# Performance work log

Measured on AMD Instinct MI355X. Metric: run time of the kernel, lower is better.

Reference implementation:

```python
import jax, jax.numpy as jnp
import numpy as np

B, N_FEAT, SEQ, E, H, V = 32, 196, 64, 1024, 1024, 32000


def setup_inputs() -> dict:
    key = jax.random.key(0)
    ks = jax.random.split(key, 16)
    s = 0.02
    return {
        "features": jax.random.normal(ks[0], (B, N_FEAT, E), jnp.float32),
        "captions": jax.random.randint(ks[1], (B, SEQ), 0, V),
        "max_seq_length": SEQ,
        # decoder embedding table (vocab, embed)
        "emb": jax.random.normal(ks[2], (V, E), jnp.float32) * s,
        # attention MLP: Linear(E->H), Tanh, Linear(H->1)
        "Wa1": jax.random.normal(ks[3], (H, E), jnp.float32) * s,
        "ba1": jnp.zeros((H,), jnp.float32),
        "Wa2": jax.random.normal(ks[4], (1, H), jnp.float32) * s,
        "ba2": jnp.zeros((1,), jnp.float32),
        # GRU (1 layer), input = concat(word_emb, context) -> E + H
        "W_ih": jax.random.normal(ks[5], (3 * H, E + H), jnp.float32) * s,
        "W_hh": jax.random.normal(ks[6], (3 * H, H), jnp.float32) * s,
        "b_ih": jnp.zeros((3 * H,), jnp.float32),
        "b_hh": jnp.zeros((3 * H,), jnp.float32),
        # output projection Linear(H -> V)
        "W_fc": jax.random.normal(ks[7], (V, H), jnp.float32) * s,
        "b_fc": jnp.zeros((V,), jnp.float32),
    }


def reference(features, captions, max_seq_length, emb, Wa1, ba1, Wa2, ba2,
              W_ih, W_hh, b_ih, b_hh, W_fc, b_fc):
    # words: (B, S, E)
    words = emb[captions]
    # combined: (B, N_FEAT + S, E)
    combined = jnp.concatenate([features, words], axis=1)
    # attention scores over the combined tokens, softmax along token axis
    scores = jnp.tanh(combined @ Wa1.T + ba1) @ Wa2.T + ba2   # (B, M, 1)
    A = jax.nn.softmax(scores, axis=1)                         # (B, M, 1)
    # context h0 = A^T @ combined -> (B, E); used both as GRU h0 and per-step context
    h0 = jnp.sum(A * combined, axis=1)
    context = h0

    def gru_cell(x, h):
        gi = x @ W_ih.T + b_ih          # (B, 3H)
        gh = h @ W_hh.T + b_hh          # (B, 3H)
        ir, iz, inn = jnp.split(gi, 3, axis=-1)
        hr, hz, hn = jnp.split(gh, 3, axis=-1)
        r = jax.nn.sigmoid(ir + hr)
        z = jax.nn.sigmoid(iz + hz)
        n = jnp.tanh(inn + r * hn)
        return (1.0 - z) * n + z * h

    def step(carry, _):
        input_word, h = carry
        x = jnp.concatenate([emb[input_word], context], axis=-1)  # (B, E+H)
        h_new = gru_cell(x, h)
        out = h_new @ W_fc.T + b_fc                               # (B, V)
        # greedy feedback (eval path / no teacher forcing)
        next_word = jnp.argmax(out, axis=-1)
        return (next_word, h_new), out

    init = (captions[:, 0], h0)
    (_, _), outs = jax.lax.scan(step, init, None, length=max_seq_length - 1)
    outs = jnp.transpose(outs, (1, 0, 2))                         # (B, S-1, V)
    bsz = captions.shape[0]
    vocab = W_fc.shape[0]
    outputs = jnp.concatenate(
        [jnp.zeros((bsz, 1, vocab), outs.dtype), outs], axis=1)   # t=0 stays zero
    return outputs, A
```

## Files before the change

kernel.cpp:

```cpp
#include <hip/hip_runtime.h>
#include <hip/hip_bf16.h>

typedef unsigned long long ull;
typedef unsigned int uint;

#define NB 32
#define NFEAT 196
#define SEQL 64
#define ED 1024
#define HD 1024
#define VOC 32000
#define NCOMB 260
#define NROWS (NB*NCOMB)
#define NTILE 2000

typedef __attribute__((ext_vector_type(8))) short s16x8;
typedef __attribute__((ext_vector_type(4))) float f32x4;
typedef __attribute__((ext_vector_type(4))) uint  u32x4;

union FragU { u32x4 u; s16x8 s; };

#define DOT4(acc, wv, xv) acc = fmaf((wv).x,(xv).x, fmaf((wv).y,(xv).y, fmaf((wv).z,(xv).z, fmaf((wv).w,(xv).w,(acc)))))

__device__ __forceinline__ uint enc_f32(float f) {
    uint u = __float_as_uint(f);
    return (u & 0x80000000u) ? ~u : (u | 0x80000000u);
}
__device__ __forceinline__ ull shflxor64(ull v, int m) {
    uint lo = __shfl_xor((uint)v, m);
    uint hi = __shfl_xor((uint)(v >> 32), m);
    return (((ull)hi) << 32) | (ull)lo;
}

__device__ __forceinline__ void split2(float a, float b, uint& hi, uint& lo) {
    __hip_bfloat162 h2 = __float22bfloat162_rn(make_float2(a, b));
    float2 hf = __bfloat1622float2(h2);
    __hip_bfloat162 l2 = __float22bfloat162_rn(make_float2(a - hf.x, b - hf.y));
    hi = *(uint*)&h2;
    lo = *(uint*)&l2;
}

__device__ __forceinline__ void nt_store4(float* p, float a, float b, float c, float d) {
    f32x4 v = {a, b, c, d};
    __builtin_nontemporal_store(v, (f32x4*)p);
}

__global__ void __launch_bounds__(256) k_build(
    const float* __restrict__ features, const int* __restrict__ captions,
    const float* __restrict__ emb, float* __restrict__ combined,
    float* __restrict__ out)
{
    const int bid = blockIdx.x;
    const int t = threadIdx.x;
    if (bid < NROWS) {
        const int b = bid / NCOMB;
        const int i = bid - b*NCOMB;
        const float* src = (i < NFEAT)
            ? (features + ((size_t)(b*NFEAT + i))*ED)
            : (emb + (size_t)captions[b*SEQL + (i - NFEAT)]*ED);
        float4* dst4 = (float4*)(combined + (size_t)bid*ED);
        const float4* s4 = (const float4*)src;
        dst4[t] = s4[t];
    } else {
        const int z = bid - NROWS;
        const int m = z*1024 + t*4;
        if (m < NB*VOC) {
            const int b = m / VOC;
            const int v = m - b*VOC;
            nt_store4(out + (size_t)b*((size_t)SEQL*VOC) + v, 0.f, 0.f, 0.f, 0.f);
        }
    }
}

__global__ void __launch_bounds__(256) k_pack_w1(
    const float* __restrict__ Wa1, uint* __restrict__ W1hi, uint* __restrict__ W1lo)
{
    const int eid = blockIdx.x*256 + threadIdx.x;
    const int lane = eid & 63;
    const int ks = (eid >> 6) & 31;
    const int ct = eid >> 11;
    const int c = ct*16 + (lane & 15);
    const int k0 = ks*32 + ((lane >> 4) & 3)*4;
    const float4 wa = *(const float4*)&Wa1[(size_t)c*ED + k0];
    const float4 wb = *(const float4*)&Wa1[(size_t)c*ED + k0 + 16];
    uint hi[4], lo[4];
    split2(wa.x, wa.y, hi[0], lo[0]);
    split2(wa.z, wa.w, hi[1], lo[1]);
    split2(wb.x, wb.y, hi[2], lo[2]);
    split2(wb.z, wb.w, hi[3], lo[3]);
    *(u32x4*)&W1hi[(size_t)eid*4] = (u32x4){hi[0], hi[1], hi[2], hi[3]};
    *(u32x4*)&W1lo[(size_t)eid*4] = (u32x4){lo[0], lo[1], lo[2], lo[3]};
}

__global__ void __launch_bounds__(256) k_pack_wfc(
    const float* __restrict__ W_fc, uint* __restrict__ Whi, uint* __restrict__ Wlo)
{
    const int eid = blockIdx.x*256 + threadIdx.x;
    const int lane = eid & 63;
    const int ks = (eid >> 6) & 31;
    const int tile = eid >> 11;
    const int row = tile*16 + (lane & 15);
    const int k0 = ks*32 + ((lane >> 4) & 3)*4;
    const float4 wa = *(const float4*)&W_fc[(size_t)row*HD + k0];
    const float4 wb = *(const float4*)&W_fc[(size_t)row*HD + k0 + 16];
    uint hi[4], lo[4];
    split2(wa.x, wa.y, hi[0], lo[0]);
    split2(wa.z, wa.w, hi[1], lo[1]);
    split2(wb.x, wb.y, hi[2], lo[2]);
    split2(wb.z, wb.w, hi[3], lo[3]);
    *(u32x4*)&Whi[(size_t)eid*4] = (u32x4){hi[0], hi[1], hi[2], hi[3]};
    *(u32x4*)&Wlo[(size_t)eid*4] = (u32x4){lo[0], lo[1], lo[2], lo[3]};
}

__global__ void __launch_bounds__(256) k_attn_mfma(
    const float* __restrict__ combined, const uint* __restrict__ W1hi,
    const uint* __restrict__ W1lo, const float* __restrict__ ba1,
    const float* __restrict__ Wa2, float* __restrict__ partials)
{
    const int t = threadIdx.x;
    const int w = t >> 6, l = t & 63;
    const int lane16 = l & 15, qk = (l >> 4) & 3;
    const int rt = blockIdx.x*4 + w;
    const int cg0 = blockIdx.y*2;

    const float* Arow = combined + (size_t)(rt*16 + lane16)*ED;
    const u32x4* bh_base = (const u32x4*)W1hi + l;
    const u32x4* bl_base = (const u32x4*)W1lo + l;

    f32x4 acc[2][4];
#pragma unroll
    for (int c = 0; c < 2; ++c)
#pragma unroll
        for (int i = 0; i < 4; ++i) acc[c][i] = (f32x4){0.f,0.f,0.f,0.f};

#pragma unroll 2
    for (int ks = 0; ks < 32; ++ks) {
        const int k0 = ks*32 + qk*4;
        const float4 aa = *(const float4*)(Arow + k0);
        const float4 ab = *(const float4*)(Arow + k0 + 16);
        FragU ahi, alo;
        uint h0,l0_,h1,l1_,h2,l2_,h3,l3_;
        split2(aa.x, aa.y, h0, l0_);
        split2(aa.z, aa.w, h1, l1_);
        split2(ab.x, ab.y, h2, l2_);
        split2(ab.z, ab.w, h3, l3_);
        ahi.u = (u32x4){h0, h1, h2, h3};
        alo.u = (u32x4){l0_, l1_, l2_, l3_};
#pragma unroll
        for (int c = 0; c < 2; ++c) {
#pragma unroll
            for (int i = 0; i < 4; ++i) {
                const size_t idx = (((size_t)((cg0 + c)*4 + i))*32 + ks)*64;
                FragU bh_, bl_;
                bh_.u = bh_base[idx];
                bl_.u = bl_base[idx];
                acc[c][i] = __builtin_amdgcn_mfma_f32_16x16x32_bf16(ahi.s, bh_.s, acc[c][i], 0, 0, 0);
                acc[c][i] = __builtin_amdgcn_mfma_f32_16x16x32_bf16(ahi.s, bl_.s, acc[c][i], 0, 0, 0);
                acc[c][i] = __builtin_amdgcn_mfma_f32_16x16x32_bf16(alo.s, bh_.s, acc[c][i], 0, 0, 0);
            }
        }
    }

#pragma unroll
    for (int c = 0; c < 2; ++c) {
        const int cg = cg0 + c;
        float s[4];
#pragma unroll
        for (int r = 0; r < 4; ++r) {
            float sum = 0.f;
#pragma unroll
            for (int i = 0; i < 4; ++i) {
                const int col = cg*64 + i*16 + lane16;
                sum += tanhf(acc[c][i][r] + ba1[col]) * Wa2[col];
            }
            s[r] = sum;
        }
#pragma unroll
        for (int m = 1; m <= 8; m <<= 1)
#pragma unroll
            for (int r = 0; r < 4; ++r) s[r] += __shfl_xor(s[r], m);
        if (lane16 == 0) {
#pragma unroll
            for (int r = 0; r < 4; ++r)
                partials[(size_t)(rt*16 + qk*4 + r)*16 + cg] = s[r];
        }
    }
}

__global__ void __launch_bounds__(256) k_attn_finish(
    const float* __restrict__ partials, const float* __restrict__ combined,
    const int* __restrict__ captions,
    float* __restrict__ A_out, float* __restrict__ h0,
    float* __restrict__ ctx, ull* __restrict__ slots0)
{
    const int b = blockIdx.x, t = threadIdx.x;
    __shared__ float sc[NCOMB];
    __shared__ float red[256];

    for (int i = t; i < NCOMB; i += 256) {
        float s = 0.f;
        const float* pr = partials + (size_t)(b*NCOMB + i)*16;
#pragma unroll
        for (int g = 0; g < 16; ++g) s += pr[g];
        sc[i] = s;
    }
    __syncthreads();
    float m = -1e30f;
    for (int i = t; i < NCOMB; i += 256) m = fmaxf(m, sc[i]);
    red[t] = m; __syncthreads();
    for (int s2 = 128; s2 > 0; s2 >>= 1) {
        if (t < s2) red[t] = fmaxf(red[t], red[t+s2]);
        __syncthreads();
    }
    m = red[0]; __syncthreads();
    float ssum = 0.f;
    for (int i = t; i < NCOMB; i += 256) { float e = expf(sc[i] - m); sc[i] = e; ssum += e; }
    red[t] = ssum; __syncthreads();
    for (int s2 = 128; s2 > 0; s2 >>= 1) {
        if (t < s2) red[t] += red[t+s2];
        __syncthreads();
    }
    const float S = red[0]; __syncthreads();
    for (int i = t; i < NCOMB; i += 256) {
        const float a = sc[i] / S;
        sc[i] = a;
        A_out[b*NCOMB + i] = a;
    }
    __syncthreads();
    for (int e = t; e < HD; e += 256) {
        float acc = 0.f;
        const float* cb = combined + (size_t)b*NCOMB*ED + e;
        for (int i = 0; i < NCOMB; ++i) acc = fmaf(sc[i], cb[(size_t)i*ED], acc);
        h0[(size_t)b*HD + e] = acc;
        ctx[(size_t)b*HD + e] = acc;
    }
    if (t == 0) {
        slots0[0*NB + b] = (ull)(~(uint)captions[b*SEQL]);
#pragma unroll
        for (int g = 1; g < 8; ++g) slots0[g*NB + b] = 0ull;
    }
}

__global__ void __launch_bounds__(256) k_gictx(
    const float* __restrict__ W_ih, const float* __restrict__ b_ih,
    const float* __restrict__ ctx, float* __restrict__ gictx)
{
    const int jj = blockIdx.x;
    const int t = threadIdx.x;
    const int w = t >> 6, l = t & 63;
    const int b0 = w*8;
    const float* Wrow = W_ih + (size_t)jj*(ED+HD) + ED;

    float a[8];
#pragma unroll
    for (int i = 0; i < 8; ++i) a[i] = 0.f;
#pragma unroll
    for (int q = 0; q < 4; ++q) {
        const int k = q*256 + l*4;
        const float4 wv = *(const float4*)(Wrow + k);
#pragma unroll
        for (int i = 0; i < 8; ++i) {
            const float4 xv = *(const float4*)(ctx + (size_t)(b0 + i)*HD + k);
            DOT4(a[i], wv, xv);
        }
    }
    int s = (l >> 5) & 1;
    int ib = s*4;
    float tA[4];
#pragma unroll
    for (int ii = 0; ii < 4; ++ii) {
        const float send = a[(1^s)*4 + ii];
        tA[ii] = a[s*4 + ii] + __shfl_xor(send, 32);
    }
    s = (l >> 4) & 1; ib += s*2;
    float tB[2];
#pragma unroll
    for (int jj2 = 0; jj2 < 2; ++jj2) {
        const float send = tA[(1^s)*2 + jj2];
        tB[jj2] = tA[s*2 + jj2] + __shfl_xor(send, 16);
    }
    s = (l >> 3) & 1; ib += s;
    float fg;
    {
        const float send = tB[1^s];
        fg = tB[s] + __shfl_xor(send, 8);
    }
#pragma unroll
    for (int mm = 4; mm >= 1; mm >>= 1) fg += __shfl_xor(fg, mm);
    if ((l & 7) == 0)
        gictx[(size_t)jj*NB + (b0 + ib)] = fg + b_ih[jj];
}

__global__ void __launch_bounds__(256) k_gru(
    const float* __restrict__ emb, const float* __restrict__ W_ih,
    const float* __restrict__ W_hh, const float* __restrict__ gictx,
    const float* __restrict__ b_hh,
    const float* __restrict__ h_prev, float* __restrict__ h_next,
    const ull* __restrict__ slots_prev, ull* __restrict__ slots_cur,
    uint* __restrict__ Hhi, uint* __restrict__ Hlo)
{
    __shared__ int word_s[NB];
    const int t = threadIdx.x;
    if (t < NB) {
        ull best = 0ull;
#pragma unroll
        for (int g = 0; g < 8; ++g) {
            ull k = slots_prev[g*NB + t];
            best = (k > best) ? k : best;
        }
        word_s[t] = (int)(~(uint)best);
    }
    if (blockIdx.x == 0) slots_cur[t] = 0ull;
    __syncthreads();

    const int j = blockIdx.x;
    const int w = t >> 6, l = t & 63;
    const int b0 = w*8;

    float a[4][8];
#pragma unroll
    for (int g = 0; g < 4; ++g)
#pragma unroll
        for (int i = 0; i < 8; ++i) a[g][i] = 0.f;

    const float* Wr = W_ih + (size_t)j*(ED+HD);
    const float* Wz = W_ih + (size_t)(HD + j)*(ED+HD);
    const float* Wn = W_ih + (size_t)(2*HD + j)*(ED+HD);
#pragma unroll
    for (int q = 0; q < 4; ++q) {
        const int k = q*256 + l*4;
        const float4 wr = *(const float4*)(Wr + k);
        const float4 wz = *(const float4*)(Wz + k);
        const float4 wn = *(const float4*)(Wn + k);
#pragma unroll
        for (int i = 0; i < 8; ++i) {
            const float4 xv = *(const float4*)(emb + (size_t)word_s[b0+i]*ED + k);
            DOT4(a[0][i], wr, xv);
            DOT4(a[1][i], wz, xv);
            DOT4(a[2][i], wn, xv);
        }
    }
    const float* Ur = W_hh + (size_t)j*HD;
    const float* Uz = W_hh + (size_t)(HD + j)*HD;
    const float* Un = W_hh + (size_t)(2*HD + j)*HD;
#pragma unroll
    for (int q = 0; q < 4; ++q) {
        const int k = q*256 + l*4;
        const float4 ur = *(const float4*)(Ur + k);
        const float4 uz = *(const float4*)(Uz + k);
        const float4 un = *(const float4*)(Un + k);
#pragma unroll
        for (int i = 0; i < 8; ++i) {
            const float4 hv = *(const float4*)(h_prev + (size_t)(b0+i)*HD + k);
            DOT4(a[0][i], ur, hv);
            DOT4(a[1][i], uz, hv);
            DOT4(a[3][i], un, hv);
        }
    }
    int s = (l >> 5) & 1;
    int ib = s*4;
    float tA[4][4];
#pragma unroll
    for (int g = 0; g < 4; ++g)
#pragma unroll
        for (int ii = 0; ii < 4; ++ii) {
            const float send = a[g][(1^s)*4 + ii];
            tA[g][ii] = a[g][s*4 + ii] + __shfl_xor(send, 32);
        }
    s = (l >> 4) & 1; ib += s*2;
    float tB[4][2];
#pragma unroll
    for (int g = 0; g < 4; ++g)
#pragma unroll
        for (int jj = 0; jj < 2; ++jj) {
            const float send = tA[g][(1^s)*2 + jj];
            tB[g][jj] = tA[g][s*2 + jj] + __shfl_xor(send, 16);
        }
    s = (l >> 3) & 1; ib += s;
    float fg[4];
#pragma unroll
    for (int g = 0; g < 4; ++g) {
        const float send = tB[g][1^s];
        fg[g] = tB[g][s] + __shfl_xor(send, 8);
    }
#pragma unroll
    for (int mm = 4; mm >= 1; mm >>= 1)
#pragma unroll
        for (int g = 0; g < 4; ++g) fg[g] += __shfl_xor(fg[g], mm);

    if ((l & 7) == 0) {
        const int b = b0 + ib;
        const float gcr = gictx[(size_t)j*NB + b];
        const float gcz = gictx[(size_t)(HD + j)*NB + b];
        const float gcn = gictx[(size_t)(2*HD + j)*NB + b];
        const float rg = 1.f/(1.f + expf(-(fg[0] + gcr + b_hh[j])));
        const float zg = 1.f/(1.f + expf(-(fg[1] + gcz + b_hh[HD+j])));
        const float ng = tanhf(fg[2] + gcn + rg*(fg[3] + b_hh[2*HD+j]));
        const float hp = h_prev[(size_t)b*HD + j];
        const float hv = (1.f - zg)*ng + zg*hp;
        h_next[(size_t)b*HD + j] = hv;
        __hip_bfloat16 hb = __float2bfloat16(hv);
        const float hf = __bfloat162float(hb);
        __hip_bfloat16 lb = __float2bfloat16(hv - hf);
        const int bh = b >> 4;
        const int ks = j >> 5;
        const int qk2 = (j >> 2) & 3;
        const int elem = (j & 3) + 4*((j >> 4) & 1);
        const size_t ei = (((size_t)(bh*32 + ks))*64 + qk2*16 + (b & 15))*8 + elem;
        ((ushort*)Hhi)[ei] = *(const ushort*)&hb;
        ((ushort*)Hlo)[ei] = *(const ushort*)&lb;
    }
}

__global__ void __launch_bounds__(256) k_logits(
    const float* __restrict__ W_fc, const uint* __restrict__ Wfchi,
    const uint* __restrict__ Wfclo, const uint* __restrict__ Hhi,
    const uint* __restrict__ Hlo, const float* __restrict__ b_fc,
    float* __restrict__ out, ull* __restrict__ slots_cur, int tstep, int packed)
{
    __shared__ float sm[32][68];
    __shared__ float mergebuf[2][64][16];
    const int t = threadIdx.x;
    const int w = t >> 6, l = t & 63;
    const int lane16 = l & 15, qk = (l >> 4) & 3;
    const int tp = w & 1;
    const int kh = w >> 1;
    const int tile0 = blockIdx.x*4 + tp*2;

    const u32x4* hh0 = (const u32x4*)Hhi + (size_t)(kh*16)*64 + l;
    const u32x4* hl0 = (const u32x4*)Hlo + (size_t)(kh*16)*64 + l;
    const u32x4* hh1 = (const u32x4*)Hhi + (size_t)(32 + kh*16)*64 + l;
    const u32x4* hl1 = (const u32x4*)Hlo + (size_t)(32 + kh*16)*64 + l;

    f32x4 accA0 = {0.f,0.f,0.f,0.f};
    f32x4 accA1 = {0.f,0.f,0.f,0.f};
    f32x4 accB0 = {0.f,0.f,0.f,0.f};
    f32x4 accB1 = {0.f,0.f,0.f,0.f};

    if (packed) {
        const u32x4* WHa = (const u32x4*)Wfchi + ((size_t)tile0*32 + kh*16)*64 + l;
        const u32x4* WLa = (const u32x4*)Wfclo + ((size_t)tile0*32 + kh*16)*64 + l;
        const u32x4* WHb = WHa + (size_t)32*64;
        const u32x4* WLb = WLa + (size_t)32*64;
#pragma unroll 2
        for (int ks = 0; ks < 16; ++ks) {
            FragU wha, wla, whb, wlb, b0h, b0l, b1h, b1l;
            wha.u = WHa[ks*64];
            wla.u = WLa[ks*64];
            whb.u = WHb[ks*64];
            wlb.u = WLb[ks*64];
            b0h.u = hh0[ks*64];
            b0l.u = hl0[ks*64];
            b1h.u = hh1[ks*64];
            b1l.u = hl1[ks*64];
            accA0 = __builtin_amdgcn_mfma_f32_16x16x32_bf16(wha.s, b0h.s, accA0, 0, 0, 0);
            accA0 = __builtin_amdgcn_mfma_f32_16x16x32_bf16(wha.s, b0l.s, accA0, 0, 0, 0);
            accA0 = __builtin_amdgcn_mfma_f32_16x16x32_bf16(wla.s, b0h.s, accA0, 0, 0, 0);
            accA1 = __builtin_amdgcn_mfma_f32_16x16x32_bf16(wha.s, b1h.s, accA1, 0, 0, 0);
            accA1 = __builtin_amdgcn_mfma_f32_16x16x32_bf16(wha.s, b1l.s, accA1, 0, 0, 0);
            accA1 = __builtin_amdgcn_mfma_f32_16x16x32_bf16(wla.s, b1h.s, accA1, 0, 0, 0);
            accB0 = __builtin_amdgcn_mfma_f32_16x16x32_bf16(whb.s, b0h.s, accB0, 0, 0, 0);
            accB0 = __builtin_amdgcn_mfma_f32_16x16x32_bf16(whb.s, b0l.s, accB0, 0, 0, 0);
            accB0 = __builtin_amdgcn_mfma_f32_16x16x32_bf16(wlb.s, b0h.s, accB0, 0, 0, 0);
            accB1 = __builtin_amdgcn_mfma_f32_16x16x32_bf16(whb.s, b1h.s, accB1, 0, 0, 0);
            accB1 = __builtin_amdgcn_mfma_f32_16x16x32_bf16(whb.s, b1l.s, accB1, 0, 0, 0);
            accB1 = __builtin_amdgcn_mfma_f32_16x16x32_bf16(wlb.s, b1h.s, accB1, 0, 0, 0);
        }
    } else {
        const float* WrowA = W_fc + (size_t)(tile0*16 + lane16)*HD;
        const float* WrowB = W_fc + (size_t)((tile0 + 1)*16 + lane16)*HD;
#pragma unroll 2
        for (int ks = 0; ks < 16; ++ks) {
            const int k0 = (kh*16 + ks)*32 + qk*4;
            const float4 waA = *(const float4*)(WrowA + k0);
            const float4 wbA = *(const float4*)(WrowA + k0 + 16);
            const float4 waB = *(const float4*)(WrowB + k0);
            const float4 wbB = *(const float4*)(WrowB + k0 + 16);
            FragU wha, wla, whb, wlb;
            uint h0,l0_,h1,l1_,h2,l2_,h3,l3_;
            split2(waA.x, waA.y, h0, l0_);
            split2(waA.z, waA.w, h1, l1_);
            split2(wbA.x, wbA.y, h2, l2_);
            split2(wbA.z, wbA.w, h3, l3_);
            wha.u = (u32x4){h0, h1, h2, h3};
            wla.u = (u32x4){l0_, l1_, l2_, l3_};
            split2(waB.x, waB.y, h0, l0_);
            split2(waB.z, waB.w, h1, l1_);
            split2(wbB.x, wbB.y, h2, l2_);
            split2(wbB.z, wbB.w, h3, l3_);
            whb.u = (u32x4){h0, h1, h2, h3};
            wlb.u = (u32x4){l0_, l1_, l2_, l3_};
            FragU b0h, b0l, b1h, b1l;
            b0h.u = hh0[ks*64];
            b0l.u = hl0[ks*64];
            b1h.u = hh1[ks*64];
            b1l.u = hl1[ks*64];
            accA0 = __builtin_amdgcn_mfma_f32_16x16x32_bf16(wha.s, b0h.s, accA0, 0, 0, 0);
            accA0 = __builtin_amdgcn_mfma_f32_16x16x32_bf16(wha.s, b0l.s, accA0, 0, 0, 0);
            accA0 = __builtin_amdgcn_mfma_f32_16x16x32_bf16(wla.s, b0h.s, accA0, 0, 0, 0);
            accA1 = __builtin_amdgcn_mfma_f32_16x16x32_bf16(wha.s, b1h.s, accA1, 0, 0, 0);
            accA1 = __builtin_amdgcn_mfma_f32_16x16x32_bf16(wha.s, b1l.s, accA1, 0, 0, 0);
            accA1 = __builtin_amdgcn_mfma_f32_16x16x32_bf16(wla.s, b1h.s, accA1, 0, 0, 0);
            accB0 = __builtin_amdgcn_mfma_f32_16x16x32_bf16(whb.s, b0h.s, accB0, 0, 0, 0);
            accB0 = __builtin_amdgcn_mfma_f32_16x16x32_bf16(whb.s, b0l.s, accB0, 0, 0, 0);
            accB0 = __builtin_amdgcn_mfma_f32_16x16x32_bf16(wlb.s, b0h.s, accB0, 0, 0, 0);
            accB1 = __builtin_amdgcn_mfma_f32_16x16x32_bf16(whb.s, b1h.s, accB1, 0, 0, 0);
            accB1 = __builtin_amdgcn_mfma_f32_16x16x32_bf16(whb.s, b1l.s, accB1, 0, 0, 0);
            accB1 = __builtin_amdgcn_mfma_f32_16x16x32_bf16(wlb.s, b1h.s, accB1, 0, 0, 0);
        }
    }

    if (kh == 1) {
        float* rr = &mergebuf[tp][l][0];
        *(float4*)&rr[0]  = make_float4(accA0[0], accA0[1], accA0[2], accA0[3]);
        *(float4*)&rr[4]  = make_float4(accA1[0], accA1[1], accA1[2], accA1[3]);
        *(float4*)&rr[8]  = make_float4(accB0[0], accB0[1], accB0[2], accB0[3]);
        *(float4*)&rr[12] = make_float4(accB1[0], accB1[1], accB1[2], accB1[3]);
    }
    __syncthreads();
    if (kh == 0) {
        const float* rr = &mergebuf[tp][l][0];
        const float4 biasA = *(const float4*)&b_fc[tile0*16 + qk*4];
        const float4 biasB = *(const float4*)&b_fc[(tile0 + 1)*16 + qk*4];
#pragma unroll
        for (int r = 0; r < 4; ++r) {
            const int rlocA = tp*32 + qk*4 + r;
            const int rlocB = tp*32 + 16 + qk*4 + r;
            const float bA = (&biasA.x)[r];
            const float bB = (&biasB.x)[r];
            sm[lane16][rlocA]      = accA0[r] + rr[r]      + bA;
            sm[16 + lane16][rlocA] = accA1[r] + rr[4 + r]  + bA;
            sm[lane16][rlocB]      = accB0[r] + rr[8 + r]  + bB;
            sm[16 + lane16][rlocB] = accB1[r] + rr[12 + r] + bB;
        }
    }
    __syncthreads();
    {
        const int b = t >> 3;
        const int rl0 = (t & 7)*8;
        const int vbase = blockIdx.x*64 + rl0;
        float v[8];
        ull bk = 0ull;
#pragma unroll
        for (int e = 0; e < 8; ++e) {
            v[e] = sm[b][rl0 + e];
            const ull key = (((ull)enc_f32(v[e])) << 32) | (ull)(~(uint)(vbase + e));
            bk = (key > bk) ? key : bk;
        }
        float* dst = out + (size_t)b*((size_t)SEQL*VOC) + (size_t)tstep*VOC + vbase;
        nt_store4(dst,     v[0], v[1], v[2], v[3]);
        nt_store4(dst + 4, v[4], v[5], v[6], v[7]);
#pragma unroll
        for (int mm = 4; mm >= 1; mm >>= 1) {
            const ull o = shflxor64(bk, mm);
            bk = (o > bk) ? o : bk;
        }
        if ((t & 7) == 0) atomicMax(slots_cur + (blockIdx.x & 7)*NB + b, bk);
    }
}

extern "C" void kernel_launch(void* const* d_in, const int* in_sizes, int n_in,
                              void* d_out, int out_size, void* d_ws, size_t ws_size,
                              hipStream_t stream)
{
    const float* features = (const float*)d_in[0];
    const int*   captions = (const int*)d_in[1];
    const float* emb  = (const float*)d_in[3];
    const float* Wa1  = (const float*)d_in[4];
    const float* ba1  = (const float*)d_in[5];
    const float* Wa2  = (const float*)d_in[6];
    const float* W_ih = (const float*)d_in[8];
    const float* W_hh = (const float*)d_in[9];
    const float* b_ih = (const float*)d_in[10];
    const float* b_hh = (const float*)d_in[11];
    const float* W_fc = (const float*)d_in[12];
    const float* b_fc = (const float*)d_in[13];

    float* out = (float*)d_out;
    float* A_out = out + (size_t)NB*SEQL*VOC;

    char* wsp = (char*)d_ws;
    float* combined = (float*)wsp;  wsp += (size_t)NROWS*ED*4;
    float* partials = (float*)wsp;  wsp += (size_t)NROWS*16*4;
    float* hbuf0    = (float*)wsp;  wsp += (size_t)NB*HD*4;
    float* hbuf1    = (float*)wsp;  wsp += (size_t)NB*HD*4;
    float* ctx      = (float*)wsp;  wsp += (size_t)NB*HD*4;
    ull*   slots    = (ull*)wsp;    wsp += 2*8*NB*sizeof(ull);
    uint*  Hhi      = (uint*)wsp;   wsp += (size_t)4096*16;
    uint*  Hlo      = (uint*)wsp;   wsp += (size_t)4096*16;
    uint*  W1hi     = (uint*)wsp;   wsp += (size_t)131072*16;
    uint*  W1lo     = (uint*)wsp;   wsp += (size_t)131072*16;
    float* gictx    = (float*)wsp;  wsp += (size_t)3*HD*NB*4;
    uint*  Wfchi    = (uint*)wsp;   wsp += (size_t)NTILE*32*64*16;
    uint*  Wfclo    = (uint*)wsp;   wsp += (size_t)NTILE*32*64*16;
    size_t packed_need = (size_t)(wsp - (char*)d_ws);
    const int packed = (ws_size >= packed_need) ? 1 : 0;

    k_build<<<NROWS + 1000, 256, 0, stream>>>(features, captions, emb, combined, out);
    k_pack_w1<<<512, 256, 0, stream>>>(Wa1, W1hi, W1lo);
    if (packed)
        k_pack_wfc<<<NTILE*32*64/256, 256, 0, stream>>>(W_fc, Wfchi, Wfclo);
    k_attn_mfma<<<dim3(130, 8), 256, 0, stream>>>(combined, W1hi, W1lo, ba1, Wa2, partials);
    k_attn_finish<<<NB, 256, 0, stream>>>(partials, combined, captions,
                                          A_out, hbuf0, ctx, slots);
    k_gictx<<<3*HD, 256, 0, stream>>>(W_ih, b_ih, ctx, gictx);
    for (int t = 1; t < SEQL; ++t) {
        const float* hp = (t & 1) ? hbuf0 : hbuf1;
        float*       hn = (t & 1) ? hbuf1 : hbuf0;
        const ull* sp = slots + (size_t)((t - 1) & 1)*8*NB;
        ull*       scur = slots + (size_t)(t & 1)*8*NB;
        k_gru<<<1024, 256, 0, stream>>>(emb, W_ih, W_hh, gictx, b_hh,
                                        hp, hn, sp, scur, Hhi, Hlo);
        k_logits<<<NTILE/4, 256, 0, stream>>>(W_fc, Wfchi, Wfclo, Hhi, Hlo, b_fc,
                                              out, scur, t, packed);
    }
}
```

Before: 3.714 ms.

## Split logits K-dimension across four waves and remap attention block tiling

The logits kernel now has each block handle two vocab tiles, with all four waves splitting the K dimension into quarters and reducing through shared memory. The grid doubles to NTILE/2 blocks so more workgroups run per step. The attention GEMM's wave-to-tile mapping changes so the four waves of a block share one row tile and each takes different column groups, which should improve reuse of A rows across waves. The trade-off is more shared-memory reduction work and half as many logits written per block.

```diff
diff --git a/kernel.cpp b/kernel.cpp
--- a/kernel.cpp
+++ b/kernel.cpp
@@ -120,8 +120,8 @@
     const int t = threadIdx.x;
     const int w = t >> 6, l = t & 63;
     const int lane16 = l & 15, qk = (l >> 4) & 3;
-    const int rt = blockIdx.x*4 + w;
-    const int cg0 = blockIdx.y*2;
+    const int rt = blockIdx.x;
+    const int cg0 = blockIdx.y*8 + w*2;
 
     const float* Arow = combined + (size_t)(rt*16 + lane16)*ED;
     const u32x4* bh_base = (const u32x4*)W1hi + l;
@@ -418,19 +418,18 @@
     const uint* __restrict__ Hlo, const float* __restrict__ b_fc,
     float* __restrict__ out, ull* __restrict__ slots_cur, int tstep, int packed)
 {
-    __shared__ float sm[32][68];
-    __shared__ float mergebuf[2][64][16];
+    __shared__ float sm[32][33];
+    __shared__ float mergebuf[3][64][16];
     const int t = threadIdx.x;
     const int w = t >> 6, l = t & 63;
     const int lane16 = l & 15, qk = (l >> 4) & 3;
-    const int tp = w & 1;
-    const int kh = w >> 1;
-    const int tile0 = blockIdx.x*4 + tp*2;
-
-    const u32x4* hh0 = (const u32x4*)Hhi + (size_t)(kh*16)*64 + l;
-    const u32x4* hl0 = (const u32x4*)Hlo + (size_t)(kh*16)*64 + l;
-    const u32x4* hh1 = (const u32x4*)Hhi + (size_t)(32 + kh*16)*64 + l;
-    const u32x4* hl1 = (const u32x4*)Hlo + (size_t)(32 + kh*16)*64 + l;
+    const int kh = w;
+    const int tile0 = blockIdx.x*2;
+
+    const u32x4* hh0 = (const u32x4*)Hhi + (size_t)(kh*8)*64 + l;
+    const u32x4* hl0 = (const u32x4*)Hlo + (size_t)(kh*8)*64 + l;
+    const u32x4* hh1 = (const u32x4*)Hhi + (size_t)(32 + kh*8)*64 + l;
+    const u32x4* hl1 = (const u32x4*)Hlo + (size_t)(32 + kh*8)*64 + l;
 
     f32x4 accA0 = {0.f,0.f,0.f,0.f};
     f32x4 accA1 = {0.f,0.f,0.f,0.f};
@@ -438,12 +437,12 @@
     f32x4 accB1 = {0.f,0.f,0.f,0.f};
 
     if (packed) {
-        const u32x4* WHa = (const u32x4*)Wfchi + ((size_t)tile0*32 + kh*16)*64 + l;
-        const u32x4* WLa = (const u32x4*)Wfclo + ((size_t)tile0*32 + kh*16)*64 + l;
+        const u32x4* WHa = (const u32x4*)Wfchi + ((size_t)tile0*32 + kh*8)*64 + l;
+        const u32x4* WLa = (const u32x4*)Wfclo + ((size_t)tile0*32 + kh*8)*64 + l;
         const u32x4* WHb = WHa + (size_t)32*64;
         const u32x4* WLb = WLa + (size_t)32*64;
 #pragma unroll 2
-        for (int ks = 0; ks < 16; ++ks) {
+        for (int ks = 0; ks < 8; ++ks) {
             FragU wha, wla, whb, wlb, b0h, b0l, b1h, b1l;
             wha.u = WHa[ks*64];
             wla.u = WLa[ks*64];
@@ -470,8 +469,8 @@
         const float* WrowA = W_fc + (size_t)(tile0*16 + lane16)*HD;
         const float* WrowB = W_fc + (size_t)((tile0 + 1)*16 + lane16)*HD;
 #pragma unroll 2
-        for (int ks = 0; ks < 16; ++ks) {
-            const int k0 = (kh*16 + ks)*32 + qk*4;
+        for (int ks = 0; ks < 8; ++ks) {
+            const int k0 = (kh*8 + ks)*32 + qk*4;
             const float4 waA = *(const float4*)(WrowA + k0);
             const float4 wbA = *(const float4*)(WrowA + k0 + 16);
             const float4 waB = *(const float4*)(WrowB + k0);
@@ -510,8 +509,8 @@
         }
     }
 
-    if (kh == 1) {
-        float* rr = &mergebuf[tp][l][0];
+    if (kh > 0) {
+        float* rr = &mergebuf[kh - 1][l][0];
         *(float4*)&rr[0]  = make_float4(accA0[0], accA0[1], accA0[2], accA0[3]);
         *(float4*)&rr[4]  = make_float4(accA1[0], accA1[1], accA1[2], accA1[3]);
         *(float4*)&rr[8]  = make_float4(accB0[0], accB0[1], accB0[2], accB0[3]);
@@ -519,43 +518,44 @@
     }
     __syncthreads();
     if (kh == 0) {
-        const float* rr = &mergebuf[tp][l][0];
+        const float* r1 = &mergebuf[0][l][0];
+        const float* r2 = &mergebuf[1][l][0];
+        const float* r3 = &mergebuf[2][l][0];
         const float4 biasA = *(const float4*)&b_fc[tile0*16 + qk*4];
         const float4 biasB = *(const float4*)&b_fc[(tile0 + 1)*16 + qk*4];
 #pragma unroll
         for (int r = 0; r < 4; ++r) {
-            const int rlocA = tp*32 + qk*4 + r;
-            const int rlocB = tp*32 + 16 + qk*4 + r;
+            const int rlocA = qk*4 + r;
+            const int rlocB = 16 + qk*4 + r;
             const float bA = (&biasA.x)[r];
             const float bB = (&biasB.x)[r];
-            sm[lane16][rlocA]      = accA0[r] + rr[r]      + bA;
-            sm[16 + lane16][rlocA] = accA1[r] + rr[4 + r]  + bA;
-            sm[lane16][rlocB]      = accB0[r] + rr[8 + r]  + bB;
-            sm[16 + lane16][rlocB] = accB1[r] + rr[12 + r] + bB;
+            sm[lane16][rlocA]      = accA0[r] + r1[r]      + r2[r]      + r3[r]      + bA;
+            sm[16 + lane16][rlocA] = accA1[r] + r1[4 + r]  + r2[4 + r]  + r3[4 + r]  + bA;
+            sm[lane16][rlocB]      = accB0[r] + r1[8 + r]  + r2[8 + r]  + r3[8 + r]  + bB;
+            sm[16 + lane16][rlocB] = accB1[r] + r1[12 + r] + r2[12 + r] + r3[12 + r] + bB;
         }
     }
     __syncthreads();
     {
         const int b = t >> 3;
-        const int rl0 = (t & 7)*8;
-        const int vbase = blockIdx.x*64 + rl0;
-        float v[8];
+        const int rq = t & 7;
+        const int vbase = blockIdx.x*32 + rq*4;
+        float v[4];
         ull bk = 0ull;
 #pragma unroll
-        for (int e = 0; e < 8; ++e) {
-            v[e] = sm[b][rl0 + e];
+        for (int e = 0; e < 4; ++e) {
+            v[e] = sm[b][rq*4 + e];
             const ull key = (((ull)enc_f32(v[e])) << 32) | (ull)(~(uint)(vbase + e));
             bk = (key > bk) ? key : bk;
         }
-        float* dst = out + (size_t)b*((size_t)SEQL*VOC) + (size_t)tstep*VOC + vbase;
-        nt_store4(dst,     v[0], v[1], v[2], v[3]);
-        nt_store4(dst + 4, v[4], v[5], v[6], v[7]);
+        nt_store4(out + (size_t)b*((size_t)SEQL*VOC) + (size_t)tstep*VOC + vbase,
+                  v[0], v[1], v[2], v[3]);
 #pragma unroll
         for (int mm = 4; mm >= 1; mm >>= 1) {
             const ull o = shflxor64(bk, mm);
             bk = (o > bk) ? o : bk;
         }
-        if ((t & 7) == 0) atomicMax(slots_cur + (blockIdx.x & 7)*NB + b, bk);
+        if (rq == 0) atomicMax(slots_cur + (blockIdx.x & 7)*NB + b, bk);
     }
 }
 
@@ -600,7 +600,7 @@
     k_pack_w1<<<512, 256, 0, stream>>>(Wa1, W1hi, W1lo);
     if (packed)
         k_pack_wfc<<<NTILE*32*64/256, 256, 0, stream>>>(W_fc, Wfchi, Wfclo);
-    k_attn_mfma<<<dim3(130, 8), 256, 0, stream>>>(combined, W1hi, W1lo, ba1, Wa2, partials);
+    k_attn_mfma<<<dim3(520, 2), 256, 0, stream>>>(combined, W1hi, W1lo, ba1, Wa2, partials);
     k_attn_finish<<<NB, 256, 0, stream>>>(partials, combined, captions,
                                           A_out, hbuf0, ctx, slots);
     k_gictx<<<3*HD, 256, 0, stream>>>(W_ih, b_ih, ctx, gictx);
@@ -611,7 +611,7 @@
         ull*       scur = slots + (size_t)(t & 1)*8*NB;
         k_gru<<<1024, 256, 0, stream>>>(emb, W_ih, W_hh, gictx, b_hh,
                                         hp, hn, sp, scur, Hhi, Hlo);
-        k_logits<<<NTILE/4, 256, 0, stream>>>(W_fc, Wfchi, Wfclo, Hhi, Hlo, b_fc,
+        k_logits<<<NTILE/2, 256, 0, stream>>>(W_fc, Wfchi, Wfclo, Hhi, Hlo, b_fc,
                                               out, scur, t, packed);
     }
 }
```

After: 3.750 ms. About the same (+1.0%).

## Overlap next-step hidden GEMV with logits kernel by moving W_hh work

Applied to the files above, without the earlier changes.

The recurrent W_hh·h product for the next step is computed inside the logits kernel launch, using extra blocks that run alongside the vocabulary projection. The GRU kernel then only does the embedding-input product and reads the precomputed gh from workspace. This shortens the serial GRU kernel on the critical path and fills idle CUs during logits. In exchange there is an extra gh buffer round-trip, and the logits kernel grid grows, with its blocks competing for bandwidth.

```diff
diff --git a/kernel.cpp b/kernel.cpp
--- a/kernel.cpp
+++ b/kernel.cpp
@@ -13,6 +13,7 @@
 #define NCOMB 260
 #define NROWS (NB*NCOMB)
 #define NTILE 2000
+#define LBLK (NTILE/4)
 
 typedef __attribute__((ext_vector_type(8))) short s16x8;
 typedef __attribute__((ext_vector_type(4))) float f32x4;
@@ -43,6 +44,73 @@
 __device__ __forceinline__ void nt_store4(float* p, float a, float b, float c, float d) {
     f32x4 v = {a, b, c, d};
     __builtin_nontemporal_store(v, (f32x4*)p);
+}
+
+__device__ __forceinline__ void gh_body(
+    int j, const float* __restrict__ W_hh, const float* __restrict__ h,
+    float* __restrict__ gh, int w, int l)
+{
+    const int b0 = w*8;
+    float a[3][8];
+#pragma unroll
+    for (int g = 0; g < 3; ++g)
+#pragma unroll
+        for (int i = 0; i < 8; ++i) a[g][i] = 0.f;
+
+    const float* Ur = W_hh + (size_t)j*HD;
+    const float* Uz = W_hh + (size_t)(HD + j)*HD;
+    const float* Un = W_hh + (size_t)(2*HD + j)*HD;
+#pragma unroll
+    for (int q = 0; q < 4; ++q) {
+        const int k = q*256 + l*4;
+        const float4 ur = *(const float4*)(Ur + k);
+        const float4 uz = *(const float4*)(Uz + k);
+        const float4 un = *(const float4*)(Un + k);
+#pragma unroll
+        for (int i = 0; i < 8; ++i) {
+            const float4 hv = *(const float4*)(h + (size_t)(b0+i)*HD + k);
+            DOT4(a[0][i], ur, hv);
+            DOT4(a[1][i], uz, hv);
+            DOT4(a[2][i], un, hv);
+        }
+    }
+    int s = (l >> 5) & 1;
+    int ib = s*4;
+    float tA[3][4];
+#pragma unroll
+    for (int g = 0; g < 3; ++g)
+#pragma unroll
+        for (int ii = 0; ii < 4; ++ii) {
+            const float send = a[g][(1^s)*4 + ii];
+            tA[g][ii] = a[g][s*4 + ii] + __shfl_xor(send, 32);
+        }
+    s = (l >> 4) & 1; ib += s*2;
+    float tB[3][2];
+#pragma unroll
+    for (int g = 0; g < 3; ++g)
+#pragma unroll
+        for (int jj = 0; jj < 2; ++jj) {
+            const float send = tA[g][(1^s)*2 + jj];
+            tB[g][jj] = tA[g][s*2 + jj] + __shfl_xor(send, 16);
+        }
+    s = (l >> 3) & 1; ib += s;
+    float fg[3];
+#pragma unroll
+    for (int g = 0; g < 3; ++g) {
+        const float send = tB[g][1^s];
+        fg[g] = tB[g][s] + __shfl_xor(send, 8);
+    }
+#pragma unroll
+    for (int mm = 4; mm >= 1; mm >>= 1)
+#pragma unroll
+        for (int g = 0; g < 3; ++g) fg[g] += __shfl_xor(fg[g], mm);
+
+    if ((l & 7) == 0) {
+        const int b = b0 + ib;
+        gh[(size_t)(0*HD + j)*NB + b] = fg[0];
+        gh[(size_t)(1*HD + j)*NB + b] = fg[1];
+        gh[(size_t)(2*HD + j)*NB + b] = fg[2];
+    }
 }
 
 __global__ void __launch_bounds__(256) k_build(
@@ -291,9 +359,17 @@
         gictx[(size_t)jj*NB + (b0 + ib)] = fg + b_ih[jj];
 }
 
-__global__ void __launch_bounds__(256) k_gru(
+__global__ void __launch_bounds__(256) k_gh(
+    const float* __restrict__ W_hh, const float* __restrict__ h,
+    float* __restrict__ gh)
+{
+    const int t = threadIdx.x;
+    gh_body(blockIdx.x, W_hh, h, gh, t >> 6, t & 63);
+}
+
+__global__ void __launch_bounds__(256) k_gru_rest(
     const float* __restrict__ emb, const float* __restrict__ W_ih,
-    const float* __restrict__ W_hh, const float* __restrict__ gictx,
+    const float* __restrict__ gh, const float* __restrict__ gictx,
     const float* __restrict__ b_hh,
     const float* __restrict__ h_prev, float* __restrict__ h_next,
     const ull* __restrict__ slots_prev, ull* __restrict__ slots_cur,
@@ -317,9 +393,9 @@
     const int w = t >> 6, l = t & 63;
     const int b0 = w*8;
 
-    float a[4][8];
-#pragma unroll
-    for (int g = 0; g < 4; ++g)
+    float a[3][8];
+#pragma unroll
+    for (int g = 0; g < 3; ++g)
 #pragma unroll
         for (int i = 0; i < 8; ++i) a[g][i] = 0.f;
 
@@ -340,62 +416,48 @@
             DOT4(a[2][i], wn, xv);
         }
     }
-    const float* Ur = W_hh + (size_t)j*HD;
-    const float* Uz = W_hh + (size_t)(HD + j)*HD;
-    const float* Un = W_hh + (size_t)(2*HD + j)*HD;
-#pragma unroll
-    for (int q = 0; q < 4; ++q) {
-        const int k = q*256 + l*4;
-        const float4 ur = *(const float4*)(Ur + k);
-        const float4 uz = *(const float4*)(Uz + k);
-        const float4 un = *(const float4*)(Un + k);
-#pragma unroll
-        for (int i = 0; i < 8; ++i) {
-            const float4 hv = *(const float4*)(h_prev + (size_t)(b0+i)*HD + k);
-            DOT4(a[0][i], ur, hv);
-            DOT4(a[1][i], uz, hv);
-            DOT4(a[3][i], un, hv);
-        }
-    }
     int s = (l >> 5) & 1;
     int ib = s*4;
-    float tA[4][4];
-#pragma unroll
-    for (int g = 0; g < 4; ++g)
+    float tA[3][4];
+#pragma unroll
+    for (int g = 0; g < 3; ++g)
 #pragma unroll
         for (int ii = 0; ii < 4; ++ii) {
             const float send = a[g][(1^s)*4 + ii];
             tA[g][ii] = a[g][s*4 + ii] + __shfl_xor(send, 32);
         }
     s = (l >> 4) & 1; ib += s*2;
-    float tB[4][2];
-#pragma unroll
-    for (int g = 0; g < 4; ++g)
+    float tB[3][2];
+#pragma unroll
+    for (int g = 0; g < 3; ++g)
 #pragma unroll
         for (int jj = 0; jj < 2; ++jj) {
             const float send = tA[g][(1^s)*2 + jj];
             tB[g][jj] = tA[g][s*2 + jj] + __shfl_xor(send, 16);
         }
     s = (l >> 3) & 1; ib += s;
-    float fg[4];
-#pragma unroll
-    for (int g = 0; g < 4; ++g) {
+    float fg[3];
+#pragma unroll
+    for (int g = 0; g < 3; ++g) {
         const float send = tB[g][1^s];
         fg[g] = tB[g][s] + __shfl_xor(send, 8);
     }
 #pragma unroll
     for (int mm = 4; mm >= 1; mm >>= 1)
 #pragma unroll
-        for (int g = 0; g < 4; ++g) fg[g] += __shfl_xor(fg[g], mm);
+        for (int g = 0; g < 3; ++g) fg[g] += __shfl_xor(fg[g], mm);
 
     if ((l & 7) == 0) {
         const int b = b0 + ib;
         const float gcr = gictx[(size_t)j*NB + b];
         const float gcz = gictx[(size_t)(HD + j)*NB + b];
         const float gcn = gictx[(size_t)(2*HD + j)*NB + b];
-        const float rg = 1.f/(1.f + expf(-(fg[0] + gcr + b_hh[j])));
-        const float zg = 1.f/(1.f + expf(-(fg[1] + gcz + b_hh[HD+j])));
-        const float ng = tanhf(fg[2] + gcn + rg*(fg[3] + b_hh[2*HD+j]));
+        const float ghr = gh[(size_t)(0*HD + j)*NB + b];
+        const float ghz = gh[(size_t)(1*HD + j)*NB + b];
+        const float ghn = gh[(size_t)(2*HD + j)*NB + b];
+        const float rg = 1.f/(1.f + expf(-(fg[0] + ghr + gcr + b_hh[j])));
+        const float zg = 1.f/(1.f + expf(-(fg[1] + ghz + gcz + b_hh[HD+j])));
+        const float ng = tanhf(fg[2] + gcn + rg*(ghn + b_hh[2*HD+j]));
         const float hp = h_prev[(size_t)b*HD + j];
         const float hv = (1.f - zg)*ng + zg*hp;
         h_next[(size_t)b*HD + j] = hv;
@@ -412,16 +474,24 @@
     }
 }
 
-__global__ void __launch_bounds__(256) k_logits(
+__global__ void __launch_bounds__(256) k_logits_gh(
     const float* __restrict__ W_fc, const uint* __restrict__ Wfchi,
     const uint* __restrict__ Wfclo, const uint* __restrict__ Hhi,
     const uint* __restrict__ Hlo, const float* __restrict__ b_fc,
-    float* __restrict__ out, ull* __restrict__ slots_cur, int tstep, int packed)
+    float* __restrict__ out, ull* __restrict__ slots_cur, int tstep, int packed,
+    const float* __restrict__ W_hh, const float* __restrict__ hcur,
+    float* __restrict__ gh)
 {
     __shared__ float sm[32][68];
     __shared__ float mergebuf[2][64][16];
     const int t = threadIdx.x;
     const int w = t >> 6, l = t & 63;
+
+    if (blockIdx.x >= LBLK) {
+        gh_body(blockIdx.x - LBLK, W_hh, hcur, gh, w, l);
+        return;
+    }
+
     const int lane16 = l & 15, qk = (l >> 4) & 3;
     const int tp = w & 1;
     const int kh = w >> 1;
@@ -591,6 +661,7 @@
     uint*  W1hi     = (uint*)wsp;   wsp += (size_t)131072*16;
     uint*  W1lo     = (uint*)wsp;   wsp += (size_t)131072*16;
     float* gictx    = (float*)wsp;  wsp += (size_t)3*HD*NB*4;
+    float* gh       = (float*)wsp;  wsp += (size_t)3*HD*NB*4;
     uint*  Wfchi    = (uint*)wsp;   wsp += (size_t)NTILE*32*64*16;
     uint*  Wfclo    = (uint*)wsp;   wsp += (size_t)NTILE*32*64*16;
     size_t packed_need = (size_t)(wsp - (char*)d_ws);
@@ -604,14 +675,16 @@
     k_attn_finish<<<NB, 256, 0, stream>>>(partials, combined, captions,
                                           A_out, hbuf0, ctx, slots);
     k_gictx<<<3*HD, 256, 0, stream>>>(W_ih, b_ih, ctx, gictx);
+    k_gh<<<HD, 256, 0, stream>>>(W_hh, hbuf0, gh);
     for (int t = 1; t < SEQL; ++t) {
         const float* hp = (t & 1) ? hbuf0 : hbuf1;
         float*       hn = (t & 1) ? hbuf1 : hbuf0;
         const ull* sp = slots + (size_t)((t - 1) & 1)*8*NB;
         ull*       scur = slots + (size_t)(t & 1)*8*NB;
-        k_gru<<<1024, 256, 0, stream>>>(emb, W_ih, W_hh, gictx, b_hh,
-                                        hp, hn, sp, scur, Hhi, Hlo);
-        k_logits<<<NTILE/4, 256, 0, stream>>>(W_fc, Wfchi, Wfclo, Hhi, Hlo, b_fc,
-                                              out, scur, t, packed);
-    }
-}
+        k_gru_rest<<<HD, 256, 0, stream>>>(emb, W_ih, gh, gictx, b_hh,
+                                           hp, hn, sp, scur, Hhi, Hlo);
+        k_logits_gh<<<LBLK + HD, 256, 0, stream>>>(W_fc, Wfchi, Wfclo, Hhi, Hlo,
+                                                   b_fc, out, scur, t, packed,
+                                                   W_hh, hn, gh);
+    }
+}
```

After: 3.660 ms (median of 2 runs). Within noise of the previous version (-1.4%).
